# Kernel tuning notes

Hardware: AMD Instinct MI355X
Metric: run time of the kernel (lower is better)

Reference implementation:

```python
import jax, jax.numpy as jnp
import numpy as np

B, DIN, DH, DOUT = 4096, 512, 1024, 256
DFF = 4 * DH
STEPS = 30
REF_DIM = 64
GAMMA = 0.5 * min(1.0, float(np.sqrt(REF_DIM / DIN)))  # dimension-scaled gamma
LN_EPS = 1e-5


def setup_inputs() -> dict:
    key = jax.random.key(0)
    ks = jax.random.split(key, 6)
    rn = lambda k, shp, s: (jax.random.normal(k, shp, jnp.float32) * s)
    return {
        "x": rn(ks[0], (B, DIN), 1.0),
        "embed_w": rn(ks[1], (DH, DIN), 0.02),
        "embed_b": jnp.zeros((DH,), jnp.float32),
        "W1": rn(ks[2], (DFF, DH), 0.02),
        "b1": jnp.zeros((DFF,), jnp.float32),
        "W2": rn(ks[3], (DH, DFF), 0.02),
        "b2": jnp.zeros((DH,), jnp.float32),
        "ln_g": jnp.ones((DH,), jnp.float32),
        "ln_b": jnp.zeros((DH,), jnp.float32),
        "head_w": rn(ks[4], (DOUT, DH), 0.02),
        "head_b": jnp.zeros((DOUT,), jnp.float32),
    }


def _spectral_normalize(W, n_iter=15):
    # power iteration (u, v treated as constants, like torch spectral_norm buffers)
    v0 = jnp.full((W.shape[1],), 1.0 / np.sqrt(W.shape[1]), W.dtype)
    def body(i, uv):
        _, v = uv
        u = W @ v
        u = u / (jnp.linalg.norm(u) + 1e-12)
        v = W.T @ u
        v = v / (jnp.linalg.norm(v) + 1e-12)
        return (u, v)
    u0 = W @ v0
    u0 = u0 / (jnp.linalg.norm(u0) + 1e-12)
    u, v = jax.lax.fori_loop(0, n_iter, body, (u0, v0))
    u = jax.lax.stop_gradient(u)
    v = jax.lax.stop_gradient(v)
    sigma = u @ (W @ v)  # grad flows through W here, as in torch
    return W / sigma


def _layernorm(h, g, b):
    mu = jnp.mean(h, axis=-1, keepdims=True)
    var = jnp.var(h, axis=-1, keepdims=True)
    return (h - mu) * jax.lax.rsqrt(var + LN_EPS) * g + b


def reference(x, embed_w, embed_b, W1, b1, W2, b2, ln_g, ln_b, head_w, head_b):
    W1n = _spectral_normalize(W1)
    W2n = _spectral_normalize(W2)
    x_emb = x @ embed_w.T + embed_b  # [B, DH]; constant across steps

    def ffn(h):
        hn = _layernorm(h, ln_g, ln_b)
        hid = jnp.tanh(hn @ W1n.T + b1)  # dropout p=0 -> identity
        return hid @ W2n.T + b2

    def step(h, _):
        h_target = ffn(h) + x_emb
        h_next = (1.0 - GAMMA) * h + GAMMA * h_target
        return h_next, None

    h, _ = jax.lax.scan(step, x_emb, None, length=STEPS)
    return h @ head_w.T + head_b
```

## Files before the change

### kernel.cpp

```cpp
#include <hip/hip_runtime.h>
#include <hip/hip_bf16.h>
#include <math.h>

#define B_    4096
#define DIN_  512
#define DH_   1024
#define DOUT_ 256
#define DFF_  4096
#define STEPS_ 30
#define GAMMA_ 0.17677669529663687f
#define LN_EPS_ 1e-5f

typedef __attribute__((ext_vector_type(8))) short short8;
typedef __attribute__((ext_vector_type(4))) float f32x4;

__device__ inline void gload_lds16(const void* g, void* l) {
  __builtin_amdgcn_global_load_lds(
      (const __attribute__((address_space(1))) unsigned int*)g,
      (__attribute__((address_space(3))) unsigned int*)l, 16, 0, 0);
}

__device__ inline float fast_tanh(float v) {
  const float e = __expf(2.f * v);
  return 1.f - 2.f * __builtin_amdgcn_rcpf(e + 1.f);
}

__device__ inline float bf2f(unsigned short u) {
  return __uint_as_float((unsigned)u << 16);
}

__global__ __launch_bounds__(512, 2) void gemm256(
    const __hip_bfloat16* __restrict__ A, const __hip_bfloat16* __restrict__ Bm,
    int M, int N, int K, int kc, int nt, const float* __restrict__ bias,
    int epi, __hip_bfloat16* __restrict__ bf16out) {
  __shared__ __align__(16) char lds[131072];
  const int tid = threadIdx.x;
  const int lane = tid & 63;
  const int wid = tid >> 6;
  const int wr = wid >> 2;
  const int wc = wid & 3;

  const int gx = gridDim.x;
  const int nwg = gx * gridDim.y;
  const int wg = blockIdx.y * gx + blockIdx.x;
  const int cpx = nwg >> 3;
  const int swz = (wg & 7) * cpx + (wg >> 3);
  const int bx = swz % gx, by = swz / gx;
  const int m0 = by * 256, n0 = bx * 256;
  const int zk = blockIdx.z * kc;

  const int scol = ((lane & 7) ^ (lane >> 3)) * 8;
  const int srow = lane >> 3;

  f32x4 acc[8][4];
  const f32x4 zero = {0.f, 0.f, 0.f, 0.f};
#pragma unroll
  for (int i = 0; i < 8; ++i)
#pragma unroll
    for (int j = 0; j < 4; ++j) acc[i][j] = zero;

  auto STG = [&](int t, int hrow, int isB) {
    if (t >= nt) return;
    const int kt = zk + t * 64;
    char* base = &lds[(t & 1) * 65536 + isB * 32768];
#pragma unroll
    for (int j = 0; j < 2; ++j) {
      const int rbase = hrow + wid * 16 + j * 8;
      const int r = rbase + srow;
      const __hip_bfloat16* s =
          isB ? Bm + (size_t)(n0 + r) * K + kt + scol
              : A + (size_t)(m0 + r) * K + kt + scol;
      gload_lds16((const void*)s, (void*)(base + rbase * 128));
    }
  };

  STG(0, 0, 1); STG(0, 128, 1); STG(0, 0, 0); STG(0, 128, 0);
  STG(1, 0, 1); STG(1, 128, 1);
  asm volatile("s_waitcnt vmcnt(0)" ::: "memory");
  __builtin_amdgcn_s_barrier();

  const int ar = lane & 15;
  const int hi = lane >> 4;
  const int a7 = ar & 7;
  const int co0 = (hi ^ a7) * 16;
  const int co1 = ((4 + hi) ^ a7) * 16;

  const char* Ab0 = &lds[0];
  const char* Bb0 = &lds[32768];
  const char* Ab1 = &lds[65536];
  const char* Bb1 = &lds[98304];
  const int arow = (wr * 128 + ar) * 128;
  const int brow = (wc * 64 + ar) * 128;

  const int niter = nt >> 1;
  for (int it = 0; it < niter; ++it) {
    const int t0 = it * 2;
    const bool lastit = (it == niter - 1);
    short8 a[4][2], b[4][2];

#pragma unroll
    for (int i = 0; i < 4; ++i) {
      a[i][0] = *(const short8*)(Ab0 + arow + i * 2048 + co0);
      a[i][1] = *(const short8*)(Ab0 + arow + i * 2048 + co1);
    }
#pragma unroll
    for (int j = 0; j < 2; ++j) {
      b[j][0] = *(const short8*)(Bb0 + brow + j * 2048 + co0);
      b[j][1] = *(const short8*)(Bb0 + brow + j * 2048 + co1);
    }
    STG(t0 + 1, 0, 0);
    asm volatile("s_waitcnt lgkmcnt(8)" ::: "memory");
    __builtin_amdgcn_sched_barrier(0);
    __builtin_amdgcn_s_barrier();
    asm volatile("s_waitcnt lgkmcnt(0)" ::: "memory");
    __builtin_amdgcn_sched_barrier(0);
    __builtin_amdgcn_s_setprio(1);
#pragma unroll
    for (int i = 0; i < 4; ++i)
#pragma unroll
      for (int j = 0; j < 2; ++j)
#pragma unroll
        for (int ks = 0; ks < 2; ++ks)
          acc[i][j] = __builtin_amdgcn_mfma_f32_16x16x32_bf16(a[i][ks], b[j][ks], acc[i][j], 0, 0, 0);
    __builtin_amdgcn_s_setprio(0);
    __builtin_amdgcn_sched_barrier(0);
    __builtin_amdgcn_s_barrier();

#pragma unroll
    for (int j = 0; j < 2; ++j) {
      b[2 + j][0] = *(const short8*)(Bb0 + brow + (2 + j) * 2048 + co0);
      b[2 + j][1] = *(const short8*)(Bb0 + brow + (2 + j) * 2048 + co1);
    }
    STG(t0 + 1, 128, 0);
    __builtin_amdgcn_sched_barrier(0);
    __builtin_amdgcn_s_barrier();
    asm volatile("s_waitcnt lgkmcnt(0)" ::: "memory");
    __builtin_amdgcn_sched_barrier(0);
    __builtin_amdgcn_s_setprio(1);
#pragma unroll
    for (int i = 0; i < 4; ++i)
#pragma unroll
      for (int j = 0; j < 2; ++j)
#pragma unroll
        for (int ks = 0; ks < 2; ++ks)
          acc[i][2 + j] = __builtin_amdgcn_mfma_f32_16x16x32_bf16(a[i][ks], b[2 + j][ks], acc[i][2 + j], 0, 0, 0);
    __builtin_amdgcn_s_setprio(0);
    __builtin_amdgcn_sched_barrier(0);
    __builtin_amdgcn_s_barrier();

#pragma unroll
    for (int i = 0; i < 4; ++i) {
      a[i][0] = *(const short8*)(Ab0 + arow + (4 + i) * 2048 + co0);
      a[i][1] = *(const short8*)(Ab0 + arow + (4 + i) * 2048 + co1);
    }
    STG(t0 + 2, 0, 1);
    __builtin_amdgcn_sched_barrier(0);
    __builtin_amdgcn_s_barrier();
    asm volatile("s_waitcnt lgkmcnt(0)" ::: "memory");
    __builtin_amdgcn_sched_barrier(0);
    __builtin_amdgcn_s_setprio(1);
#pragma unroll
    for (int i = 0; i < 4; ++i)
#pragma unroll
      for (int j = 0; j < 2; ++j)
#pragma unroll
        for (int ks = 0; ks < 2; ++ks)
          acc[4 + i][2 + j] = __builtin_amdgcn_mfma_f32_16x16x32_bf16(a[i][ks], b[2 + j][ks], acc[4 + i][2 + j], 0, 0, 0);
    __builtin_amdgcn_s_setprio(0);
    __builtin_amdgcn_sched_barrier(0);
    __builtin_amdgcn_s_barrier();

    STG(t0 + 2, 128, 1);
    if (lastit) {
      asm volatile("s_waitcnt vmcnt(0)" ::: "memory");
    } else {
      asm volatile("s_waitcnt vmcnt(4)" ::: "memory");
    }
    __builtin_amdgcn_sched_barrier(0);
    __builtin_amdgcn_s_barrier();
    __builtin_amdgcn_s_setprio(1);
#pragma unroll
    for (int i = 0; i < 4; ++i)
#pragma unroll
      for (int j = 0; j < 2; ++j)
#pragma unroll
        for (int ks = 0; ks < 2; ++ks)
          acc[4 + i][j] = __builtin_amdgcn_mfma_f32_16x16x32_bf16(a[i][ks], b[j][ks], acc[4 + i][j], 0, 0, 0);
    __builtin_amdgcn_s_setprio(0);
    __builtin_amdgcn_sched_barrier(0);
    __builtin_amdgcn_s_barrier();

#pragma unroll
    for (int i = 0; i < 4; ++i) {
      a[i][0] = *(const short8*)(Ab1 + arow + i * 2048 + co0);
      a[i][1] = *(const short8*)(Ab1 + arow + i * 2048 + co1);
    }
#pragma unroll
    for (int j = 0; j < 2; ++j) {
      b[j][0] = *(const short8*)(Bb1 + brow + j * 2048 + co0);
      b[j][1] = *(const short8*)(Bb1 + brow + j * 2048 + co1);
    }
    STG(t0 + 2, 0, 0);
    asm volatile("s_waitcnt lgkmcnt(8)" ::: "memory");
    __builtin_amdgcn_sched_barrier(0);
    __builtin_amdgcn_s_barrier();
    asm volatile("s_waitcnt lgkmcnt(0)" ::: "memory");
    __builtin_amdgcn_sched_barrier(0);
    __builtin_amdgcn_s_setprio(1);
#pragma unroll
    for (int i = 0; i < 4; ++i)
#pragma unroll
      for (int j = 0; j < 2; ++j)
#pragma unroll
        for (int ks = 0; ks < 2; ++ks)
          acc[i][j] = __builtin_amdgcn_mfma_f32_16x16x32_bf16(a[i][ks], b[j][ks], acc[i][j], 0, 0, 0);
    __builtin_amdgcn_s_setprio(0);
    __builtin_amdgcn_sched_barrier(0);
    __builtin_amdgcn_s_barrier();

#pragma unroll
    for (int j = 0; j < 2; ++j) {
      b[2 + j][0] = *(const short8*)(Bb1 + brow + (2 + j) * 2048 + co0);
      b[2 + j][1] = *(const short8*)(Bb1 + brow + (2 + j) * 2048 + co1);
    }
    STG(t0 + 2, 128, 0);
    __builtin_amdgcn_sched_barrier(0);
    __builtin_amdgcn_s_barrier();
    asm volatile("s_waitcnt lgkmcnt(0)" ::: "memory");
    __builtin_amdgcn_sched_barrier(0);
    __builtin_amdgcn_s_setprio(1);
#pragma unroll
    for (int i = 0; i < 4; ++i)
#pragma unroll
      for (int j = 0; j < 2; ++j)
#pragma unroll
        for (int ks = 0; ks < 2; ++ks)
          acc[i][2 + j] = __builtin_amdgcn_mfma_f32_16x16x32_bf16(a[i][ks], b[2 + j][ks], acc[i][2 + j], 0, 0, 0);
    __builtin_amdgcn_s_setprio(0);
    __builtin_amdgcn_sched_barrier(0);
    __builtin_amdgcn_s_barrier();

#pragma unroll
    for (int i = 0; i < 4; ++i) {
      a[i][0] = *(const short8*)(Ab1 + arow + (4 + i) * 2048 + co0);
      a[i][1] = *(const short8*)(Ab1 + arow + (4 + i) * 2048 + co1);
    }
    STG(t0 + 3, 0, 1);
    __builtin_amdgcn_sched_barrier(0);
    __builtin_amdgcn_s_barrier();
    asm volatile("s_waitcnt lgkmcnt(0)" ::: "memory");
    __builtin_amdgcn_sched_barrier(0);
    __builtin_amdgcn_s_setprio(1);
#pragma unroll
    for (int i = 0; i < 4; ++i)
#pragma unroll
      for (int j = 0; j < 2; ++j)
#pragma unroll
        for (int ks = 0; ks < 2; ++ks)
          acc[4 + i][2 + j] = __builtin_amdgcn_mfma_f32_16x16x32_bf16(a[i][ks], b[2 + j][ks], acc[4 + i][2 + j], 0, 0, 0);
    __builtin_amdgcn_s_setprio(0);
    __builtin_amdgcn_sched_barrier(0);
    __builtin_amdgcn_s_barrier();

    STG(t0 + 3, 128, 1);
    asm volatile("s_waitcnt vmcnt(4)" ::: "memory");
    __builtin_amdgcn_sched_barrier(0);
    __builtin_amdgcn_s_barrier();
    __builtin_amdgcn_s_setprio(1);
#pragma unroll
    for (int i = 0; i < 4; ++i)
#pragma unroll
      for (int j = 0; j < 2; ++j)
#pragma unroll
        for (int ks = 0; ks < 2; ++ks)
          acc[4 + i][j] = __builtin_amdgcn_mfma_f32_16x16x32_bf16(a[i][ks], b[j][ks], acc[4 + i][j], 0, 0, 0);
    __builtin_amdgcn_s_setprio(0);
    __builtin_amdgcn_sched_barrier(0);
    __builtin_amdgcn_s_barrier();
  }

  if (epi == 4) bf16out += (size_t)blockIdx.z * ((size_t)M * N);
  const int rb = hi * 4;
#pragma unroll
  for (int mf = 0; mf < 8; ++mf) {
#pragma unroll
    for (int nf = 0; nf < 4; ++nf) {
      const int col = n0 + wc * 64 + nf * 16 + ar;
      const float bvs = bias ? bias[col] : 0.f;
#pragma unroll
      for (int j = 0; j < 4; ++j) {
        const int row = m0 + wr * 128 + mf * 16 + rb + j;
        float v = acc[mf][nf][j] + bvs;
        if (epi == 1) v = fast_tanh(v);
        bf16out[(size_t)row * N + col] = __float2bfloat16(v);
      }
    }
  }
}

__global__ __launch_bounds__(256) void gemm_bt(
    const __hip_bfloat16* __restrict__ A, const __hip_bfloat16* __restrict__ Bm,
    int M, int N, int K, const float* __restrict__ bias, int epi,
    float* __restrict__ f32out, float* __restrict__ f32out2) {
  __shared__ __align__(16) short As[128 * 32];
  __shared__ __align__(16) short Bs[128 * 32];
  const int tid = threadIdx.x;
  const int lane = tid & 63;
  const int wid = tid >> 6;
  const int wr = wid >> 1, wc = wid & 1;

  const int gx = gridDim.x;
  const int nwg = gx * gridDim.y;
  const int wg = blockIdx.y * gx + blockIdx.x;
  const int cpx = nwg >> 3;
  const int swz = (wg & 7) * cpx + (wg >> 3);
  const int bx = swz % gx, by = swz / gx;

  const int m0 = by * 128, n0 = bx * 128;
  const int ldsrow = lane >> 2;
  const int col8 = (lane & 3) * 8;

  f32x4 acc[4][4];
  const f32x4 zero = {0.f, 0.f, 0.f, 0.f};
#pragma unroll
  for (int i = 0; i < 4; ++i)
#pragma unroll
    for (int j = 0; j < 4; ++j) acc[i][j] = zero;

  for (int kt = 0; kt < K; kt += 32) {
#pragma unroll
    for (int i = 0; i < 2; ++i) {
      const int seg = wid * 2 + i;
      gload_lds16(A + (size_t)(m0 + seg * 16 + ldsrow) * K + kt + col8,
                  (void*)(As + seg * 512));
      gload_lds16(Bm + (size_t)(n0 + seg * 16 + ldsrow) * K + kt + col8,
                  (void*)(Bs + seg * 512));
    }
    __syncthreads();
    short8 a[4], b[4];
#pragma unroll
    for (int mf = 0; mf < 4; ++mf)
      a[mf] = *(const short8*)&As[(wr * 64 + mf * 16 + (lane & 15)) * 32 + (lane >> 4) * 8];
#pragma unroll
    for (int nf = 0; nf < 4; ++nf)
      b[nf] = *(const short8*)&Bs[(wc * 64 + nf * 16 + (lane & 15)) * 32 + (lane >> 4) * 8];
#pragma unroll
    for (int mf = 0; mf < 4; ++mf)
#pragma unroll
      for (int nf = 0; nf < 4; ++nf)
        acc[mf][nf] = __builtin_amdgcn_mfma_f32_16x16x32_bf16(a[mf], b[nf], acc[mf][nf], 0, 0, 0);
    __syncthreads();
  }

  const int rbase = (lane >> 4) * 4;
  const int cin = lane & 15;
#pragma unroll
  for (int mf = 0; mf < 4; ++mf) {
#pragma unroll
    for (int nf = 0; nf < 4; ++nf) {
      const int col = n0 + wc * 64 + nf * 16 + cin;
      const float bv = bias[col];
#pragma unroll
      for (int j = 0; j < 4; ++j) {
        const int row = m0 + wr * 64 + mf * 16 + rbase + j;
        const float v = acc[mf][nf][j] + bv;
        const size_t idx = (size_t)row * N + col;
        if (epi == 0) {
          f32out[idx] = v;
          f32out2[idx] = v;
        } else {
          f32out[idx] = v;
        }
      }
    }
  }
}

__global__ __launch_bounds__(256) void reduce_ln_kernel(
    const __hip_bfloat16* __restrict__ ps, const float* __restrict__ b2,
    const float* __restrict__ xe, float* __restrict__ h,
    const float* __restrict__ g, const float* __restrict__ be,
    __hip_bfloat16* __restrict__ outbf, int do_ln) {
  const int row = blockIdx.x, tid = threadIdx.x;
  const size_t base = (size_t)row * DH_;
  const size_t slab = (size_t)B_ * DH_;
  float pv0 = 0.f, pv1 = 0.f, pv2 = 0.f, pv3 = 0.f;
#pragma unroll
  for (int z = 0; z < 4; ++z) {
    const ushort4 q = ((const ushort4*)(ps + z * slab + base))[tid];
    pv0 += bf2f(q.x); pv1 += bf2f(q.y); pv2 += bf2f(q.z); pv3 += bf2f(q.w);
  }
  const float4 xv = ((const float4*)(xe + base))[tid];
  const float4 hv = ((const float4*)(h + base))[tid];
  const float4 bv = ((const float4*)b2)[tid];
  float4 nv;
  nv.x = (1.f - GAMMA_) * hv.x + GAMMA_ * (pv0 + bv.x + xv.x);
  nv.y = (1.f - GAMMA_) * hv.y + GAMMA_ * (pv1 + bv.y + xv.y);
  nv.z = (1.f - GAMMA_) * hv.z + GAMMA_ * (pv2 + bv.z + xv.z);
  nv.w = (1.f - GAMMA_) * hv.w + GAMMA_ * (pv3 + bv.w + xv.w);
  ((float4*)(h + base))[tid] = nv;

  __hip_bfloat16* out = outbf + base + tid * 4;
  if (!do_ln) {
    out[0] = __float2bfloat16(nv.x);
    out[1] = __float2bfloat16(nv.y);
    out[2] = __float2bfloat16(nv.z);
    out[3] = __float2bfloat16(nv.w);
    return;
  }
  float s = nv.x + nv.y + nv.z + nv.w;
  float ss = nv.x * nv.x + nv.y * nv.y + nv.z * nv.z + nv.w * nv.w;
#pragma unroll
  for (int o = 32; o > 0; o >>= 1) {
    s += __shfl_down(s, o, 64);
    ss += __shfl_down(ss, o, 64);
  }
  __shared__ float rs_[4], rss_[4];
  const int lane = tid & 63, wid = tid >> 6;
  if (lane == 0) { rs_[wid] = s; rss_[wid] = ss; }
  __syncthreads();
  const float tot = rs_[0] + rs_[1] + rs_[2] + rs_[3];
  const float tots = rss_[0] + rss_[1] + rss_[2] + rss_[3];
  const float mu = tot * (1.f / DH_);
  const float var = tots * (1.f / DH_) - mu * mu;
  const float rstd = rsqrtf(var + LN_EPS_);
  const float4 gv = ((const float4*)g)[tid];
  const float4 bev = ((const float4*)be)[tid];
  out[0] = __float2bfloat16((nv.x - mu) * rstd * gv.x + bev.x);
  out[1] = __float2bfloat16((nv.y - mu) * rstd * gv.y + bev.y);
  out[2] = __float2bfloat16((nv.z - mu) * rstd * gv.z + bev.z);
  out[3] = __float2bfloat16((nv.w - mu) * rstd * gv.w + bev.w);
}

__global__ __launch_bounds__(256) void ln_cast_kernel(
    const float* __restrict__ h, const float* __restrict__ g,
    const float* __restrict__ be, __hip_bfloat16* __restrict__ hn) {
  const int row = blockIdx.x;
  const int tid = threadIdx.x;
  const float4 v = ((const float4*)(h + (size_t)row * DH_))[tid];
  float s = v.x + v.y + v.z + v.w;
  float ss = v.x * v.x + v.y * v.y + v.z * v.z + v.w * v.w;
#pragma unroll
  for (int o = 32; o > 0; o >>= 1) {
    s += __shfl_down(s, o, 64);
    ss += __shfl_down(ss, o, 64);
  }
  __shared__ float rs_[4], rss_[4];
  const int lane = tid & 63, wid = tid >> 6;
  if (lane == 0) { rs_[wid] = s; rss_[wid] = ss; }
  __syncthreads();
  const float tot = rs_[0] + rs_[1] + rs_[2] + rs_[3];
  const float tots = rss_[0] + rss_[1] + rss_[2] + rss_[3];
  const float mu = tot * (1.f / DH_);
  const float var = tots * (1.f / DH_) - mu * mu;
  const float rstd = rsqrtf(var + LN_EPS_);
  const float4 gv = ((const float4*)g)[tid];
  const float4 bv = ((const float4*)be)[tid];
  __hip_bfloat16* out = hn + (size_t)row * DH_ + tid * 4;
  out[0] = __float2bfloat16((v.x - mu) * rstd * gv.x + bv.x);
  out[1] = __float2bfloat16((v.y - mu) * rstd * gv.y + bv.y);
  out[2] = __float2bfloat16((v.z - mu) * rstd * gv.z + bv.z);
  out[3] = __float2bfloat16((v.w - mu) * rstd * gv.w + bv.w);
}

__global__ __launch_bounds__(256) void matvec2_kernel(
    const float* __restrict__ Wa, const float* __restrict__ xa,
    float* __restrict__ ya, int rowsA, int colsA,
    const float* __restrict__ Wb, const float* __restrict__ xb,
    float* __restrict__ yb, int rowsB, int colsB) {
  const int gw = (int)(blockIdx.x * 256 + threadIdx.x) >> 6;
  const int lane = threadIdx.x & 63;
  const float* W;
  const float* x;
  float* y;
  int row, cols;
  if (gw < rowsA) {
    W = Wa; x = xa; y = ya; row = gw; cols = colsA;
  } else {
    row = gw - rowsA;
    if (row >= rowsB) return;
    W = Wb; x = xb; y = yb; cols = colsB;
  }
  const float4* wr = (const float4*)(W + (size_t)row * cols);
  const float4* xv = (const float4*)x;
  const int n4 = cols >> 2;
  float s = 0.f;
  for (int c = lane; c < n4; c += 64) {
    const float4 wv = wr[c];
    const float4 vv = xv[c];
    s += wv.x * vv.x + wv.y * vv.y + wv.z * vv.z + wv.w * vv.w;
  }
#pragma unroll
  for (int o = 32; o > 0; o >>= 1) s += __shfl_down(s, o, 64);
  if (lane == 0) y[row] = s;
}

__global__ __launch_bounds__(256) void transpose_kernel(
    const float* __restrict__ in, float* __restrict__ out, int R, int C) {
  __shared__ float t[32][33];
  const int lx = threadIdx.x & 31, ly = threadIdx.x >> 5;
  const int r0 = blockIdx.y * 32, c0 = blockIdx.x * 32;
#pragma unroll
  for (int j = 0; j < 32; j += 8) t[ly + j][lx] = in[(size_t)(r0 + ly + j) * C + c0 + lx];
  __syncthreads();
#pragma unroll
  for (int j = 0; j < 32; j += 8) out[(size_t)(c0 + ly + j) * R + r0 + lx] = t[lx][ly + j];
}

__global__ void init_v_kernel(float* v1, float* v2) {
  const int i = blockIdx.x * 256 + threadIdx.x;
  if (i < 1024) v1[i] = 0.03125f;
  if (i < 4096) v2[i] = 0.015625f;
}

__global__ __launch_bounds__(256) void cast_kernel(
    const float* __restrict__ s, __hip_bfloat16* __restrict__ d, int n) {
  const int b = (blockIdx.x * 256 + threadIdx.x) * 4;
  if (b < n) {
    const float4 v = *(const float4*)(s + b);
    d[b] = __float2bfloat16(v.x);
    d[b + 1] = __float2bfloat16(v.y);
    d[b + 2] = __float2bfloat16(v.z);
    d[b + 3] = __float2bfloat16(v.w);
  }
}

__global__ __launch_bounds__(256) void cast_scaled_kernel(
    const float* __restrict__ s, __hip_bfloat16* __restrict__ d, int n,
    const float* __restrict__ rs) {
  const float r = rs[0];
  const int b = (blockIdx.x * 256 + threadIdx.x) * 4;
  if (b < n) {
    const float4 v = *(const float4*)(s + b);
    d[b] = __float2bfloat16(v.x * r);
    d[b + 1] = __float2bfloat16(v.y * r);
    d[b + 2] = __float2bfloat16(v.z * r);
    d[b + 3] = __float2bfloat16(v.w * r);
  }
}

__global__ __launch_bounds__(256) void sigma_rs_kernel(
    const float* __restrict__ c, int m, const float* __restrict__ dv, int n,
    float* __restrict__ rs) {
  const int tid = threadIdx.x;
  float sc = 0.f, sd = 0.f;
  for (int i = tid; i < m; i += 256) { const float v = c[i]; sc += v * v; }
  for (int i = tid; i < n; i += 256) { const float v = dv[i]; sd += v * v; }
#pragma unroll
  for (int o = 32; o > 0; o >>= 1) {
    sc += __shfl_down(sc, o, 64);
    sd += __shfl_down(sd, o, 64);
  }
  __shared__ float a[4], b[4];
  const int lane = tid & 63, wid = tid >> 6;
  if (lane == 0) { a[wid] = sc; b[wid] = sd; }
  __syncthreads();
  if (tid == 0) {
    const float tc = a[0] + a[1] + a[2] + a[3];
    const float td = b[0] + b[1] + b[2] + b[3];
    rs[0] = sqrtf(tc / td);
  }
}

extern "C" void kernel_launch(void* const* d_in, const int* in_sizes, int n_in,
                              void* d_out, int out_size, void* d_ws, size_t ws_size,
                              hipStream_t stream) {
  const float* x       = (const float*)d_in[0];
  const float* embed_w = (const float*)d_in[1];
  const float* embed_b = (const float*)d_in[2];
  const float* W1      = (const float*)d_in[3];
  const float* b1      = (const float*)d_in[4];
  const float* W2      = (const float*)d_in[5];
  const float* b2      = (const float*)d_in[6];
  const float* ln_g    = (const float*)d_in[7];
  const float* ln_b    = (const float*)d_in[8];
  const float* head_w  = (const float*)d_in[9];
  const float* head_b  = (const float*)d_in[10];
  float* out = (float*)d_out;

  char* p = (char*)d_ws;
  auto carve = [&](size_t bytes) {
    char* r = p;
    p += (bytes + 255) & ~(size_t)255;
    return (void*)r;
  };
  float* h     = (float*)carve((size_t)B_ * DH_ * 4);
  float* x_emb = (float*)carve((size_t)B_ * DH_ * 4);
  float* W1T   = (float*)carve((size_t)DFF_ * DH_ * 4);
  float* W2T   = (float*)carve((size_t)DH_ * DFF_ * 4);
  __hip_bfloat16* ps = (__hip_bfloat16*)W1T;
  __hip_bfloat16* hn   = (__hip_bfloat16*)carve((size_t)B_ * DH_ * 2);
  __hip_bfloat16* hid  = (__hip_bfloat16*)carve((size_t)B_ * DFF_ * 2);
  __hip_bfloat16* W1n  = (__hip_bfloat16*)carve((size_t)DFF_ * DH_ * 2);
  __hip_bfloat16* W2n  = (__hip_bfloat16*)carve((size_t)DH_ * DFF_ * 2);
  __hip_bfloat16* xbf  = (__hip_bfloat16*)carve((size_t)B_ * DIN_ * 2);
  __hip_bfloat16* ewbf = (__hip_bfloat16*)carve((size_t)DH_ * DIN_ * 2);
  __hip_bfloat16* hwbf = (__hip_bfloat16*)carve((size_t)DOUT_ * DH_ * 2);
  __hip_bfloat16* hbf  = (__hip_bfloat16*)carve((size_t)B_ * DH_ * 2);
  float* v1a = (float*)carve(4096 * 4);
  float* v1b = (float*)carve(4096 * 4);
  float* c1  = (float*)carve(4096 * 4);
  float* v2a = (float*)carve(4096 * 4);
  float* v2b = (float*)carve(4096 * 4);
  float* c2  = (float*)carve(4096 * 4);
  float* rs1 = (float*)carve(256);
  float* rs2 = (float*)carve(256);

  transpose_kernel<<<dim3(DH_ / 32, DFF_ / 32), 256, 0, stream>>>(W1, W1T, DFF_, DH_);
  transpose_kernel<<<dim3(DFF_ / 32, DH_ / 32), 256, 0, stream>>>(W2, W2T, DH_, DFF_);
  init_v_kernel<<<16, 256, 0, stream>>>(v1a, v2a);
  cast_kernel<<<(B_ * DIN_ / 4) / 256, 256, 0, stream>>>(x, xbf, B_ * DIN_);
  cast_kernel<<<(DH_ * DIN_ / 4) / 256, 256, 0, stream>>>(embed_w, ewbf, DH_ * DIN_);
  cast_kernel<<<(DOUT_ * DH_ / 4) / 256, 256, 0, stream>>>(head_w, hwbf, DOUT_ * DH_);

  gemm_bt<<<dim3(DH_ / 128, B_ / 128), 256, 0, stream>>>(
      xbf, ewbf, B_, DH_, DIN_, embed_b, 0, x_emb, h);

  for (int it = 0; it < 15; ++it) {
    const float* vin1 = (it & 1) ? v1b : v1a;
    float* vout1 = (it & 1) ? v1a : v1b;
    const float* vin2 = (it & 1) ? v2b : v2a;
    float* vout2 = (it & 1) ? v2a : v2b;
    matvec2_kernel<<<((DFF_ + DH_) * 64) / 256, 256, 0, stream>>>(
        W1, vin1, c1, DFF_, DH_, W2, vin2, c2, DH_, DFF_);
    matvec2_kernel<<<((DH_ + DFF_) * 64) / 256, 256, 0, stream>>>(
        W1T, c1, vout1, DH_, DFF_, W2T, c2, vout2, DFF_, DH_);
  }
  sigma_rs_kernel<<<1, 256, 0, stream>>>(c1, DFF_, v1b, DH_, rs1);
  sigma_rs_kernel<<<1, 256, 0, stream>>>(c2, DH_, v2b, DFF_, rs2);
  cast_scaled_kernel<<<(DFF_ * DH_ / 4) / 256, 256, 0, stream>>>(W1, W1n, DFF_ * DH_, rs1);
  cast_scaled_kernel<<<(DH_ * DFF_ / 4) / 256, 256, 0, stream>>>(W2, W2n, DH_ * DFF_, rs2);

  ln_cast_kernel<<<B_, 256, 0, stream>>>(h, ln_g, ln_b, hn);

  for (int s = 0; s < STEPS_; ++s) {
    gemm256<<<dim3(DFF_ / 256, B_ / 256, 1), 512, 0, stream>>>(
        hn, W1n, B_, DFF_, DH_, DH_, DH_ / 64, b1, 1, hid);
    gemm256<<<dim3(DH_ / 256, B_ / 256, 4), 512, 0, stream>>>(
        hid, W2n, B_, DH_, DFF_, DFF_ / 4, DFF_ / 4 / 64, nullptr, 4, ps);
    const int last = (s == STEPS_ - 1);
    reduce_ln_kernel<<<B_, 256, 0, stream>>>(
        ps, b2, x_emb, h, ln_g, ln_b, last ? hbf : hn, last ? 0 : 1);
  }

  gemm_bt<<<dim3(DOUT_ / 128, B_ / 128), 256, 0, stream>>>(
      hbf, hwbf, B_, DOUT_, DH_, head_b, 3, out, nullptr);
}
```

Before: 3.268 ms.

## Prefetch B fragments across pipeline stages and store x_emb as bf16

The first B-fragment pair of each LDS buffer is now loaded during the previous compute stage, using persistent pb0/pb1 registers. This lets the first MFMA block of each half-iteration start with only the A reads outstanding, and the per-stage LDS reads are split into smaller groups with a lower lgkmcnt wait. Separately, x_emb is kept in bf16 instead of fp32, which halves its read traffic in the per-step reduce kernel. The costs are higher register pressure and lower precision of the constant x_emb term.

```diff
diff --git a/kernel.cpp b/kernel.cpp
--- a/kernel.cpp
+++ b/kernel.cpp
@@ -92,24 +92,48 @@
   const int arow = (wr * 128 + ar) * 128;
   const int brow = (wc * 64 + ar) * 128;
 
+  short8 pb0[2][2], pb1[2][2];
+#pragma unroll
+  for (int j = 0; j < 2; ++j) {
+    pb0[j][0] = *(const short8*)(Bb0 + brow + j * 2048 + co0);
+    pb0[j][1] = *(const short8*)(Bb0 + brow + j * 2048 + co1);
+  }
+
   const int niter = nt >> 1;
   for (int it = 0; it < niter; ++it) {
     const int t0 = it * 2;
     const bool lastit = (it == niter - 1);
-    short8 a[4][2], b[4][2];
+    short8 a[4][2], b23[2][2];
 
 #pragma unroll
     for (int i = 0; i < 4; ++i) {
       a[i][0] = *(const short8*)(Ab0 + arow + i * 2048 + co0);
       a[i][1] = *(const short8*)(Ab0 + arow + i * 2048 + co1);
     }
+    STG(t0 + 1, 0, 0);
+    asm volatile("s_waitcnt lgkmcnt(4)" ::: "memory");
+    __builtin_amdgcn_sched_barrier(0);
+    __builtin_amdgcn_s_barrier();
+    asm volatile("s_waitcnt lgkmcnt(0)" ::: "memory");
+    __builtin_amdgcn_sched_barrier(0);
+    __builtin_amdgcn_s_setprio(1);
+#pragma unroll
+    for (int i = 0; i < 4; ++i)
+#pragma unroll
+      for (int j = 0; j < 2; ++j)
+#pragma unroll
+        for (int ks = 0; ks < 2; ++ks)
+          acc[i][j] = __builtin_amdgcn_mfma_f32_16x16x32_bf16(a[i][ks], pb0[j][ks], acc[i][j], 0, 0, 0);
+    __builtin_amdgcn_s_setprio(0);
+    __builtin_amdgcn_sched_barrier(0);
+    __builtin_amdgcn_s_barrier();
+
 #pragma unroll
     for (int j = 0; j < 2; ++j) {
-      b[j][0] = *(const short8*)(Bb0 + brow + j * 2048 + co0);
-      b[j][1] = *(const short8*)(Bb0 + brow + j * 2048 + co1);
-    }
-    STG(t0 + 1, 0, 0);
-    asm volatile("s_waitcnt lgkmcnt(8)" ::: "memory");
+      b23[j][0] = *(const short8*)(Bb0 + brow + (2 + j) * 2048 + co0);
+      b23[j][1] = *(const short8*)(Bb0 + brow + (2 + j) * 2048 + co1);
+    }
+    STG(t0 + 1, 128, 0);
     __builtin_amdgcn_sched_barrier(0);
     __builtin_amdgcn_s_barrier();
     asm volatile("s_waitcnt lgkmcnt(0)" ::: "memory");
@@ -121,29 +145,7 @@
       for (int j = 0; j < 2; ++j)
 #pragma unroll
         for (int ks = 0; ks < 2; ++ks)
-          acc[i][j] = __builtin_amdgcn_mfma_f32_16x16x32_bf16(a[i][ks], b[j][ks], acc[i][j], 0, 0, 0);
-    __builtin_amdgcn_s_setprio(0);
-    __builtin_amdgcn_sched_barrier(0);
-    __builtin_amdgcn_s_barrier();
-
-#pragma unroll
-    for (int j = 0; j < 2; ++j) {
-      b[2 + j][0] = *(const short8*)(Bb0 + brow + (2 + j) * 2048 + co0);
-      b[2 + j][1] = *(const short8*)(Bb0 + brow + (2 + j) * 2048 + co1);
-    }
-    STG(t0 + 1, 128, 0);
-    __builtin_amdgcn_sched_barrier(0);
-    __builtin_amdgcn_s_barrier();
-    asm volatile("s_waitcnt lgkmcnt(0)" ::: "memory");
-    __builtin_amdgcn_sched_barrier(0);
-    __builtin_amdgcn_s_setprio(1);
-#pragma unroll
-    for (int i = 0; i < 4; ++i)
-#pragma unroll
-      for (int j = 0; j < 2; ++j)
-#pragma unroll
-        for (int ks = 0; ks < 2; ++ks)
-          acc[i][2 + j] = __builtin_amdgcn_mfma_f32_16x16x32_bf16(a[i][ks], b[2 + j][ks], acc[i][2 + j], 0, 0, 0);
+          acc[i][2 + j] = __builtin_amdgcn_mfma_f32_16x16x32_bf16(a[i][ks], b23[j][ks], acc[i][2 + j], 0, 0, 0);
     __builtin_amdgcn_s_setprio(0);
     __builtin_amdgcn_sched_barrier(0);
     __builtin_amdgcn_s_barrier();
@@ -165,7 +167,7 @@
       for (int j = 0; j < 2; ++j)
 #pragma unroll
         for (int ks = 0; ks < 2; ++ks)
-          acc[4 + i][2 + j] = __builtin_amdgcn_mfma_f32_16x16x32_bf16(a[i][ks], b[2 + j][ks], acc[4 + i][2 + j], 0, 0, 0);
+          acc[4 + i][2 + j] = __builtin_amdgcn_mfma_f32_16x16x32_bf16(a[i][ks], b23[j][ks], acc[4 + i][2 + j], 0, 0, 0);
     __builtin_amdgcn_s_setprio(0);
     __builtin_amdgcn_sched_barrier(0);
     __builtin_amdgcn_s_barrier();
@@ -178,14 +180,19 @@
     }
     __builtin_amdgcn_sched_barrier(0);
     __builtin_amdgcn_s_barrier();
-    __builtin_amdgcn_s_setprio(1);
-#pragma unroll
-    for (int i = 0; i < 4; ++i)
-#pragma unroll
-      for (int j = 0; j < 2; ++j)
-#pragma unroll
-        for (int ks = 0; ks < 2; ++ks)
-          acc[4 + i][j] = __builtin_amdgcn_mfma_f32_16x16x32_bf16(a[i][ks], b[j][ks], acc[4 + i][j], 0, 0, 0);
+#pragma unroll
+    for (int j = 0; j < 2; ++j) {
+      pb1[j][0] = *(const short8*)(Bb1 + brow + j * 2048 + co0);
+      pb1[j][1] = *(const short8*)(Bb1 + brow + j * 2048 + co1);
+    }
+    __builtin_amdgcn_s_setprio(1);
+#pragma unroll
+    for (int i = 0; i < 4; ++i)
+#pragma unroll
+      for (int j = 0; j < 2; ++j)
+#pragma unroll
+        for (int ks = 0; ks < 2; ++ks)
+          acc[4 + i][j] = __builtin_amdgcn_mfma_f32_16x16x32_bf16(a[i][ks], pb0[j][ks], acc[4 + i][j], 0, 0, 0);
     __builtin_amdgcn_s_setprio(0);
     __builtin_amdgcn_sched_barrier(0);
     __builtin_amdgcn_s_barrier();
@@ -195,13 +202,30 @@
       a[i][0] = *(const short8*)(Ab1 + arow + i * 2048 + co0);
       a[i][1] = *(const short8*)(Ab1 + arow + i * 2048 + co1);
     }
+    STG(t0 + 2, 0, 0);
+    asm volatile("s_waitcnt lgkmcnt(4)" ::: "memory");
+    __builtin_amdgcn_sched_barrier(0);
+    __builtin_amdgcn_s_barrier();
+    asm volatile("s_waitcnt lgkmcnt(0)" ::: "memory");
+    __builtin_amdgcn_sched_barrier(0);
+    __builtin_amdgcn_s_setprio(1);
+#pragma unroll
+    for (int i = 0; i < 4; ++i)
+#pragma unroll
+      for (int j = 0; j < 2; ++j)
+#pragma unroll
+        for (int ks = 0; ks < 2; ++ks)
+          acc[i][j] = __builtin_amdgcn_mfma_f32_16x16x32_bf16(a[i][ks], pb1[j][ks], acc[i][j], 0, 0, 0);
+    __builtin_amdgcn_s_setprio(0);
+    __builtin_amdgcn_sched_barrier(0);
+    __builtin_amdgcn_s_barrier();
+
 #pragma unroll
     for (int j = 0; j < 2; ++j) {
-      b[j][0] = *(const short8*)(Bb1 + brow + j * 2048 + co0);
-      b[j][1] = *(const short8*)(Bb1 + brow + j * 2048 + co1);
-    }
-    STG(t0 + 2, 0, 0);
-    asm volatile("s_waitcnt lgkmcnt(8)" ::: "memory");
+      b23[j][0] = *(const short8*)(Bb1 + brow + (2 + j) * 2048 + co0);
+      b23[j][1] = *(const short8*)(Bb1 + brow + (2 + j) * 2048 + co1);
+    }
+    STG(t0 + 2, 128, 0);
     __builtin_amdgcn_sched_barrier(0);
     __builtin_amdgcn_s_barrier();
     asm volatile("s_waitcnt lgkmcnt(0)" ::: "memory");
@@ -213,29 +237,7 @@
       for (int j = 0; j < 2; ++j)
 #pragma unroll
         for (int ks = 0; ks < 2; ++ks)
-          acc[i][j] = __builtin_amdgcn_mfma_f32_16x16x32_bf16(a[i][ks], b[j][ks], acc[i][j], 0, 0, 0);
-    __builtin_amdgcn_s_setprio(0);
-    __builtin_amdgcn_sched_barrier(0);
-    __builtin_amdgcn_s_barrier();
-
-#pragma unroll
-    for (int j = 0; j < 2; ++j) {
-      b[2 + j][0] = *(const short8*)(Bb1 + brow + (2 + j) * 2048 + co0);
-      b[2 + j][1] = *(const short8*)(Bb1 + brow + (2 + j) * 2048 + co1);
-    }
-    STG(t0 + 2, 128, 0);
-    __builtin_amdgcn_sched_barrier(0);
-    __builtin_amdgcn_s_barrier();
-    asm volatile("s_waitcnt lgkmcnt(0)" ::: "memory");
-    __builtin_amdgcn_sched_barrier(0);
-    __builtin_amdgcn_s_setprio(1);
-#pragma unroll
-    for (int i = 0; i < 4; ++i)
-#pragma unroll
-      for (int j = 0; j < 2; ++j)
-#pragma unroll
-        for (int ks = 0; ks < 2; ++ks)
-          acc[i][2 + j] = __builtin_amdgcn_mfma_f32_16x16x32_bf16(a[i][ks], b[2 + j][ks], acc[i][2 + j], 0, 0, 0);
+          acc[i][2 + j] = __builtin_amdgcn_mfma_f32_16x16x32_bf16(a[i][ks], b23[j][ks], acc[i][2 + j], 0, 0, 0);
     __builtin_amdgcn_s_setprio(0);
     __builtin_amdgcn_sched_barrier(0);
     __builtin_amdgcn_s_barrier();
@@ -257,7 +259,7 @@
       for (int j = 0; j < 2; ++j)
 #pragma unroll
         for (int ks = 0; ks < 2; ++ks)
-          acc[4 + i][2 + j] = __builtin_amdgcn_mfma_f32_16x16x32_bf16(a[i][ks], b[2 + j][ks], acc[4 + i][2 + j], 0, 0, 0);
+          acc[4 + i][2 + j] = __builtin_amdgcn_mfma_f32_16x16x32_bf16(a[i][ks], b23[j][ks], acc[4 + i][2 + j], 0, 0, 0);
     __builtin_amdgcn_s_setprio(0);
     __builtin_amdgcn_sched_barrier(0);
     __builtin_amdgcn_s_barrier();
@@ -266,14 +268,19 @@
     asm volatile("s_waitcnt vmcnt(4)" ::: "memory");
     __builtin_amdgcn_sched_barrier(0);
     __builtin_amdgcn_s_barrier();
-    __builtin_amdgcn_s_setprio(1);
-#pragma unroll
-    for (int i = 0; i < 4; ++i)
-#pragma unroll
-      for (int j = 0; j < 2; ++j)
-#pragma unroll
-        for (int ks = 0; ks < 2; ++ks)
-          acc[4 + i][j] = __builtin_amdgcn_mfma_f32_16x16x32_bf16(a[i][ks], b[j][ks], acc[4 + i][j], 0, 0, 0);
+#pragma unroll
+    for (int j = 0; j < 2; ++j) {
+      pb0[j][0] = *(const short8*)(Bb0 + brow + j * 2048 + co0);
+      pb0[j][1] = *(const short8*)(Bb0 + brow + j * 2048 + co1);
+    }
+    __builtin_amdgcn_s_setprio(1);
+#pragma unroll
+    for (int i = 0; i < 4; ++i)
+#pragma unroll
+      for (int j = 0; j < 2; ++j)
+#pragma unroll
+        for (int ks = 0; ks < 2; ++ks)
+          acc[4 + i][j] = __builtin_amdgcn_mfma_f32_16x16x32_bf16(a[i][ks], pb1[j][ks], acc[4 + i][j], 0, 0, 0);
     __builtin_amdgcn_s_setprio(0);
     __builtin_amdgcn_sched_barrier(0);
     __builtin_amdgcn_s_barrier();
@@ -301,7 +308,7 @@
 __global__ __launch_bounds__(256) void gemm_bt(
     const __hip_bfloat16* __restrict__ A, const __hip_bfloat16* __restrict__ Bm,
     int M, int N, int K, const float* __restrict__ bias, int epi,
-    float* __restrict__ f32out, float* __restrict__ f32out2) {
+    float* __restrict__ f32out, __hip_bfloat16* __restrict__ bf16out) {
   __shared__ __align__(16) short As[128 * 32];
   __shared__ __align__(16) short Bs[128 * 32];
   const int tid = threadIdx.x;
@@ -365,12 +372,8 @@
         const int row = m0 + wr * 64 + mf * 16 + rbase + j;
         const float v = acc[mf][nf][j] + bv;
         const size_t idx = (size_t)row * N + col;
-        if (epi == 0) {
-          f32out[idx] = v;
-          f32out2[idx] = v;
-        } else {
-          f32out[idx] = v;
-        }
+        f32out[idx] = v;
+        if (epi == 0) bf16out[idx] = __float2bfloat16(v);
       }
     }
   }
@@ -378,7 +381,7 @@
 
 __global__ __launch_bounds__(256) void reduce_ln_kernel(
     const __hip_bfloat16* __restrict__ ps, const float* __restrict__ b2,
-    const float* __restrict__ xe, float* __restrict__ h,
+    const __hip_bfloat16* __restrict__ xe, float* __restrict__ h,
     const float* __restrict__ g, const float* __restrict__ be,
     __hip_bfloat16* __restrict__ outbf, int do_ln) {
   const int row = blockIdx.x, tid = threadIdx.x;
@@ -390,14 +393,14 @@
     const ushort4 q = ((const ushort4*)(ps + z * slab + base))[tid];
     pv0 += bf2f(q.x); pv1 += bf2f(q.y); pv2 += bf2f(q.z); pv3 += bf2f(q.w);
   }
-  const float4 xv = ((const float4*)(xe + base))[tid];
+  const ushort4 xq = ((const ushort4*)(xe + base))[tid];
   const float4 hv = ((const float4*)(h + base))[tid];
   const float4 bv = ((const float4*)b2)[tid];
   float4 nv;
-  nv.x = (1.f - GAMMA_) * hv.x + GAMMA_ * (pv0 + bv.x + xv.x);
-  nv.y = (1.f - GAMMA_) * hv.y + GAMMA_ * (pv1 + bv.y + xv.y);
-  nv.z = (1.f - GAMMA_) * hv.z + GAMMA_ * (pv2 + bv.z + xv.z);
-  nv.w = (1.f - GAMMA_) * hv.w + GAMMA_ * (pv3 + bv.w + xv.w);
+  nv.x = (1.f - GAMMA_) * hv.x + GAMMA_ * (pv0 + bv.x + bf2f(xq.x));
+  nv.y = (1.f - GAMMA_) * hv.y + GAMMA_ * (pv1 + bv.y + bf2f(xq.y));
+  nv.z = (1.f - GAMMA_) * hv.z + GAMMA_ * (pv2 + bv.z + bf2f(xq.z));
+  nv.w = (1.f - GAMMA_) * hv.w + GAMMA_ * (pv3 + bv.w + bf2f(xq.w));
   ((float4*)(h + base))[tid] = nv;
 
   __hip_bfloat16* out = outbf + base + tid * 4;
@@ -584,11 +587,11 @@
     p += (bytes + 255) & ~(size_t)255;
     return (void*)r;
   };
-  float* h     = (float*)carve((size_t)B_ * DH_ * 4);
-  float* x_emb = (float*)carve((size_t)B_ * DH_ * 4);
+  float* h = (float*)carve((size_t)B_ * DH_ * 4);
   float* W1T   = (float*)carve((size_t)DFF_ * DH_ * 4);
   float* W2T   = (float*)carve((size_t)DH_ * DFF_ * 4);
   __hip_bfloat16* ps = (__hip_bfloat16*)W1T;
+  __hip_bfloat16* xebf = (__hip_bfloat16*)carve((size_t)B_ * DH_ * 2);
   __hip_bfloat16* hn   = (__hip_bfloat16*)carve((size_t)B_ * DH_ * 2);
   __hip_bfloat16* hid  = (__hip_bfloat16*)carve((size_t)B_ * DFF_ * 2);
   __hip_bfloat16* W1n  = (__hip_bfloat16*)carve((size_t)DFF_ * DH_ * 2);
@@ -614,7 +617,7 @@
   cast_kernel<<<(DOUT_ * DH_ / 4) / 256, 256, 0, stream>>>(head_w, hwbf, DOUT_ * DH_);
 
   gemm_bt<<<dim3(DH_ / 128, B_ / 128), 256, 0, stream>>>(
-      xbf, ewbf, B_, DH_, DIN_, embed_b, 0, x_emb, h);
+      xbf, ewbf, B_, DH_, DIN_, embed_b, 0, h, xebf);
 
   for (int it = 0; it < 15; ++it) {
     const float* vin1 = (it & 1) ? v1b : v1a;
@@ -640,7 +643,7 @@
         hid, W2n, B_, DH_, DFF_, DFF_ / 4, DFF_ / 4 / 64, nullptr, 4, ps);
     const int last = (s == STEPS_ - 1);
     reduce_ln_kernel<<<B_, 256, 0, stream>>>(
-        ps, b2, x_emb, h, ln_g, ln_b, last ? hbf : hn, last ? 0 : 1);
+        ps, b2, xebf, h, ln_g, ln_b, last ? hbf : hn, last ? 0 : 1);
   }
 
   gemm_bt<<<dim3(DOUT_ / 128, B_ / 128), 256, 0, stream>>>(
```

Result: no change. 3.216 ms (-1.6%).
